# Kernel optimization log

Hardware: AMD Instinct MI355X
Metric: run time of the kernel (lower is better)

The kernel has to match this reference:

```python
import jax, jax.numpy as jnp
import numpy as np

B, L, H = 64, 512, 400          # batch, seq_len, encoder hidden (HeadSentinel(400))
EN, EL, NLAB = 256, 128, 128    # edge-node dim, edge-label hidden, num head_tags


def setup_inputs():
    key = jax.random.key(0)
    ks = jax.random.split(key, 16)
    g = lambda k, shape, s=0.05: jax.random.normal(k, shape, jnp.float32) * s
    return dict(
        memory_bank=jax.random.normal(ks[0], (B, L, H), jnp.float32),
        edge_heads=jax.random.randint(ks[1], (B, L), 0, L + 1, jnp.int32),
        edge_labels=jax.random.randint(ks[2], (B, L), 0, NLAB, jnp.int32),
        corefs=jax.random.randint(ks[3], (B, L), 0, L, jnp.int32),
        mask=jnp.ones((B, L), jnp.int32),
        sentinel=g(ks[4], (H,)),
        W_enh=g(ks[5], (H, EN)), b_enh=jnp.zeros((EN,), jnp.float32),
        W_enm=g(ks[6], (H, EN)), b_enm=jnp.zeros((EN,), jnp.float32),
        W_elh=g(ks[7], (H, EL)), b_elh=jnp.zeros((EL,), jnp.float32),
        W_elm=g(ks[8], (H, EL)), b_elm=jnp.zeros((EL,), jnp.float32),
        ba_U=g(ks[9], (EN, EN)), ba_Wd=g(ks[10], (EN,)), ba_We=g(ks[11], (EN,)),
        ba_b=jnp.zeros((), jnp.float32),
        lbl_U=g(ks[12], (NLAB, EL, EL)), lbl_Wl=g(ks[13], (NLAB, EL)),
        lbl_Wr=g(ks[14], (NLAB, EL)), lbl_b=jnp.zeros((NLAB,), jnp.float32),
    )


def _label_scores(elh_sel, elm, lbl_U, lbl_Wl, lbl_Wr, lbl_b):
    # Bilinear label scorer: [B, L1, NLAB]
    return (jnp.einsum('bld,nde,ble->bln', elh_sel, lbl_U, elm)
            + elh_sel @ lbl_Wl.T + elm @ lbl_Wr.T + lbl_b)


def reference(memory_bank, edge_heads, edge_labels, corefs, mask, sentinel,
              W_enh, b_enh, W_enm, b_enm, W_elh, b_elh, W_elm, b_elm,
              ba_U, ba_Wd, ba_We, ba_b, lbl_U, lbl_Wl, lbl_Wr, lbl_b):
    elu = jax.nn.elu
    Bsz = memory_bank.shape[0]
    # ---- add head sentinel (mask/heads/labels get a leading zero column) ----
    mb = jnp.concatenate([jnp.broadcast_to(sentinel, (Bsz, 1, sentinel.shape[0])), memory_bank], 1)
    z = jnp.zeros((Bsz, 1), jnp.int32)
    heads1 = jnp.concatenate([z, edge_heads], 1)    # [B, L1]
    labels1 = jnp.concatenate([z, edge_labels], 1)  # [B, L1]
    mask1 = jnp.concatenate([z, mask], 1)           # [B, L1]
    L1 = mb.shape[1]
    # ---- encode (Dropout is identity at inference) ----
    enh = elu(mb @ W_enh + b_enh)
    enm = elu(mb @ W_enm + b_enm)
    elh = elu(mb @ W_elh + b_elh)
    elm = elu(mb @ W_elm + b_elm)
    # ---- biaffine edge-node scores: s[b, head, mod] ----
    node_scores = (jnp.einsum('bhd,de,bme->bhm', enh, ba_U, enm)
                   + (enh @ ba_Wd)[:, :, None] + (enm @ ba_We)[:, None, :] + ba_b)
    # ---- loss ----
    mask2 = (mask1[:, :, None] + mask1[:, None, :]).astype(jnp.float32)
    node_ll = jax.nn.log_softmax(node_scores + jnp.log(mask2 + 1e-45), axis=1)
    elh_gold = jnp.take_along_axis(elh, heads1[:, :, None], axis=1)  # gather_nd(create_indices)
    lbl_ll = jax.nn.log_softmax(_label_scores(elh_gold, elm, lbl_U, lbl_Wl, lbl_Wr, lbl_b), axis=2)
    gold_node_ll = jnp.take_along_axis(node_ll, heads1[:, None, :], axis=1)[:, 0, :]  # ll[b, head[b,m], m]
    gold_lbl_ll = jnp.take_along_axis(lbl_ll, labels1[:, :, None], axis=2)[:, :, 0]   # ll[b, m, label[b,m]]
    node_nll = -jnp.sum(gold_node_ll[:, 1:])
    label_nll = -jnp.sum(gold_lbl_ll[:, 1:])
    # ---- decode ----
    dec = node_scores + jnp.diag(jnp.full((L1,), -jnp.inf))
    mm = (1.0 - mask1.astype(jnp.float32)) * (-1e8)
    dec = dec + mm[:, :, None] + mm[:, None, :]
    pred_heads = jnp.argmax(dec, axis=1)                              # [B, L1]
    elh_pred = jnp.take_along_axis(elh, pred_heads[:, :, None], axis=1)
    pred_lbl = jnp.max(_label_scores(elh_pred, elm, lbl_U, lbl_Wl, lbl_Wr, lbl_b), axis=2)
    return (pred_heads[:, 1:].astype(jnp.float32), pred_lbl[:, 1:],
            labels1.astype(jnp.float32), node_nll, label_nll)
```

## Files before the change

### kernel.cpp

```cpp
#include <hip/hip_runtime.h>
#include <hip/hip_bf16.h>

#define BB 64
#define LLEN 512
#define HH 400
#define L1 513
#define TT 32832
#define NE 768
#define KP 16640
#define PHW 4160
#define KPAD 416

typedef __attribute__((ext_vector_type(4))) float f32x4;
typedef __attribute__((ext_vector_type(8))) short bf16x8;
typedef unsigned int u32;
typedef __attribute__((address_space(1))) const u32* gptr_t;
typedef __attribute__((address_space(3))) u32* sptr_t;

__device__ inline unsigned short f2bf(float x){
  unsigned u = __float_as_uint(x);
  unsigned r = (u + 0x7fffu + ((u >> 16) & 1u)) >> 16;
  return (unsigned short)r;
}
__device__ inline unsigned cvtpk(float a, float b){
  unsigned r;
  asm("v_cvt_pk_bf16_f32 %0, %1, %2" : "=v"(r) : "v"(a), "v"(b));
  return r;
}
__device__ inline float bf2f(unsigned short h){
  return __uint_as_float(((unsigned)h) << 16);
}

__global__ __launch_bounds__(256) void k_init(const int* eh, const int* el, float* out,
                                              int* idx, int* labbuf){
  int t = blockIdx.x*256 + threadIdx.x;
  if (t < TT){
    int b = t / L1, m = t - b*L1;
    int lab = m ? el[b*LLEN + m - 1] : 0;
    int hd  = m ? eh[b*LLEN + m - 1] : 0;
    out[65536 + t] = (float)lab;
    labbuf[t] = lab;
    idx[t] = b*L1 + hd;
  }
  if (blockIdx.x == 0 && threadIdx.x < 2) out[98368 + threadIdx.x] = 0.f;
}

__global__ __launch_bounds__(256) void k_wcat(const float* Wenh,const float* benh,
    const float* Wenm,const float* benm,const float* Welh,const float* belh,
    const float* Welm,const float* belm, unsigned short* WH, unsigned short* WL,
    float* bcat){
  int g = blockIdx.x*256 + threadIdx.x;
  if (g < NE*KPAD){
    int n = g / KPAD, k = g - n*KPAD;
    float v = 0.f;
    if (k < HH){
      if (n < 256) v = Wenh[k*256 + n];
      else if (n < 512) v = Wenm[k*256 + n - 256];
      else if (n < 640) v = Welh[k*128 + n - 512];
      else v = Welm[k*128 + n - 640];
    }
    unsigned short h = f2bf(v);
    WH[g] = h;
    WL[g] = f2bf(v - bf2f(h));
  }
  if (g < NE){
    float v;
    if (g < 256) v = benh[g];
    else if (g < 512) v = benm[g - 256];
    else if (g < 640) v = belh[g - 512];
    else v = belm[g - 640];
    bcat[g] = v;
  }
}

__global__ __launch_bounds__(256) void k_wtt(const float* lblU, const float* Wl,
    const float* Wr, unsigned short* WtTp){
  int n = blockIdx.y;
  int kp = blockIdx.x*256 + threadIdx.x;
  if (kp >= KP) return;
  int p = kp / PHW; int q2 = kp - p*PHW; int dd = q2 >> 5; int j = q2 & 31; int e = p*32 + j;
  float v;
  if (dd < 128) v = lblU[(size_t)n*16384 + dd*128 + e];
  else if (dd == 128) v = Wl[n*128 + e];
  else v = Wr[n*128 + e];
  WtTp[(size_t)n*KP + kp] = f2bf(v);
}

#define INNER8(AS, BS) \
  _Pragma("unroll") \
  for (int kk = 0; kk < 8; kk++){ \
    float4 a0 = *(const float4*)&AS[kk][ty*8]; \
    float4 a1 = *(const float4*)&AS[kk][ty*8+4]; \
    float4 b0 = *(const float4*)&BS[kk][tx*8]; \
    float4 b1 = *(const float4*)&BS[kk][tx*8+4]; \
    float avv[8] = {a0.x,a0.y,a0.z,a0.w,a1.x,a1.y,a1.z,a1.w}; \
    float bvv[8] = {b0.x,b0.y,b0.z,b0.w,b1.x,b1.y,b1.z,b1.w}; \
    _Pragma("unroll") \
    for (int ii = 0; ii < 8; ii++) \
      _Pragma("unroll") \
      for (int jj = 0; jj < 8; jj++) \
        c_[ii][jj] += avv[ii]*bvv[jj]; \
  }

__global__ __launch_bounds__(512) void k_encm(const float* mb, const float* sent,
    const unsigned short* WH, const unsigned short* WL, const float* bcat, float* E){
  __shared__ __align__(16) unsigned char Bst[2][2][8192];
  int tid = threadIdx.x, w = tid >> 6, lane = tid & 63, c = lane & 15, q = lane >> 4;
  int tb0 = blockIdx.x*256 + w*32;
  int n0 = blockIdx.y*128;

  const float* ap[2];
  #pragma unroll
  for (int ms = 0; ms < 2; ms++){
    int row = tb0 + ms*16 + c;
    const float* p = sent;
    if (row < TT){
      int br = row / L1, mr = row - br*L1;
      if (mr) p = mb + (size_t)(br*LLEN + mr - 1)*HH;
    }
    ap[ms] = p;
  }

  int f = tid;
  int bn = ((f >> 6) << 4) + (f & 15);
  int bkq = (f >> 4) & 3;
  const char* srcH = (const char*)WH + (size_t)(n0 + bn)*(KPAD*2) + bkq*16;
  const char* srcL = (const char*)WL + (size_t)(n0 + bn)*(KPAD*2) + bkq*16;
  auto stageB = [&](int s){
    __builtin_amdgcn_global_load_lds((gptr_t)(srcH + (size_t)s*64),
        (sptr_t)(&Bst[s & 1][0][f*16]), 16, 0, 0);
    __builtin_amdgcn_global_load_lds((gptr_t)(srcL + (size_t)s*64),
        (sptr_t)(&Bst[s & 1][1][f*16]), 16, 0, 0);
  };

  float4 a0[2], a1[2];
  auto loadA = [&](int s){
    #pragma unroll
    for (int ms = 0; ms < 2; ms++){
      int k = s*32 + q*8;
      float4 v0 = make_float4(0.f,0.f,0.f,0.f), v1 = v0;
      if (k < HH){ v0 = *(const float4*)(ap[ms] + k); v1 = *(const float4*)(ap[ms] + k + 4); }
      a0[ms] = v0; a1[ms] = v1;
    }
  };
  stageB(0);
  loadA(0);

  f32x4 acc[2][8];
  #pragma unroll
  for (int ms = 0; ms < 2; ms++)
    #pragma unroll
    for (int ns = 0; ns < 8; ns++){ acc[ms][ns][0]=0.f; acc[ms][ns][1]=0.f; acc[ms][ns][2]=0.f; acc[ms][ns][3]=0.f; }

  for (int s = 0; s < 13; s++){
    asm volatile("s_waitcnt vmcnt(0)" ::: "memory");
    __builtin_amdgcn_sched_barrier(0);
    __builtin_amdgcn_s_barrier();
    __builtin_amdgcn_sched_barrier(0);
    if (s + 1 < 13) stageB(s + 1);
    bf16x8 Ah[2], Al[2];
    #pragma unroll
    for (int ms = 0; ms < 2; ms++){
      float v[8] = {a0[ms].x,a0[ms].y,a0[ms].z,a0[ms].w,a1[ms].x,a1[ms].y,a1[ms].z,a1[ms].w};
      union { unsigned u[4]; bf16x8 b; } uh, ul;
      float r[8];
      #pragma unroll
      for (int j = 0; j < 4; j++){
        unsigned h = cvtpk(v[2*j], v[2*j+1]);
        uh.u[j] = h;
        r[2*j]   = v[2*j]   - __uint_as_float((h & 0xffffu) << 16);
        r[2*j+1] = v[2*j+1] - __uint_as_float((h >> 16) << 16);
      }
      #pragma unroll
      for (int j = 0; j < 4; j++) ul.u[j] = cvtpk(r[2*j], r[2*j+1]);
      Ah[ms] = uh.b; Al[ms] = ul.b;
    }
    if (s + 1 < 13) loadA(s + 1);
    const char* bh = (const char*)&Bst[s & 1][0][0];
    const char* bl = (const char*)&Bst[s & 1][1][0];
    #pragma unroll
    for (int ns = 0; ns < 8; ns++){
      bf16x8 BH = *(const bf16x8*)(bh + ns*1024 + lane*16);
      bf16x8 BL = *(const bf16x8*)(bl + ns*1024 + lane*16);
      #pragma unroll
      for (int ms = 0; ms < 2; ms++){
        acc[ms][ns] = __builtin_amdgcn_mfma_f32_16x16x32_bf16(Ah[ms], BH, acc[ms][ns], 0, 0, 0);
        acc[ms][ns] = __builtin_amdgcn_mfma_f32_16x16x32_bf16(Ah[ms], BL, acc[ms][ns], 0, 0, 0);
        acc[ms][ns] = __builtin_amdgcn_mfma_f32_16x16x32_bf16(Al[ms], BH, acc[ms][ns], 0, 0, 0);
      }
    }
  }

  float bvv[8];
  #pragma unroll
  for (int ns = 0; ns < 8; ns++) bvv[ns] = bcat[n0 + ns*16 + c];
  #pragma unroll
  for (int ms = 0; ms < 2; ms++){
    #pragma unroll
    for (int i = 0; i < 4; i++){
      int row = tb0 + ms*16 + 4*q + i;
      if (row < TT){
        #pragma unroll
        for (int ns = 0; ns < 8; ns++){
          float t = acc[ms][ns][i] + bvv[ns];
          E[(size_t)row*NE + n0 + ns*16 + c] = t > 0.f ? t : expm1f(t);
        }
      }
    }
  }
}

__global__ __launch_bounds__(256) void k_t1(const float* E, const float* baU, float* T1){
  __shared__ float As[8][132];
  __shared__ float Bs[8][132];
  int tid = threadIdx.x, tx = tid & 15, ty = tid >> 4;
  int Mb = blockIdx.x * 128, n0 = blockIdx.y * 128;
  int ar = tid >> 1, akc = (tid & 1) * 4;
  int row = Mb + ar;
  bool aval = row < TT;
  const float* ap = E + (size_t)(aval ? row : 0)*NE;
  int bkr = tid >> 5, bnc = (tid & 31) * 4;
  float c_[8][8] = {};
  for (int k0 = 0; k0 < 256; k0 += 8){
    __syncthreads();
    float4 av = make_float4(0.f,0.f,0.f,0.f);
    if (aval) av = *(const float4*)(ap + k0 + akc);
    As[akc+0][ar] = av.x; As[akc+1][ar] = av.y; As[akc+2][ar] = av.z; As[akc+3][ar] = av.w;
    *(float4*)&Bs[bkr][bnc] = *(const float4*)(baU + (size_t)(k0 + bkr)*256 + n0 + bnc);
    __syncthreads();
    INNER8(As, Bs)
  }
  #pragma unroll
  for (int i = 0; i < 8; i++){
    int rr = Mb + ty*8 + i;
    if (rr < TT){
      float4 o0 = {c_[i][0],c_[i][1],c_[i][2],c_[i][3]};
      float4 o1 = {c_[i][4],c_[i][5],c_[i][6],c_[i][7]};
      *(float4*)&T1[(size_t)rr*256 + n0 + tx*8] = o0;
      *(float4*)&T1[(size_t)rr*256 + n0 + tx*8 + 4] = o1;
    }
  }
}

__global__ __launch_bounds__(256) void k_vecs(const float* E, const float* Wd,
    const float* We, const float* bab, float* dvec, float* evec){
  int w = threadIdx.x >> 6, lane = threadIdx.x & 63;
  int t = blockIdx.x*4 + w;
  const float* enh = E + (size_t)t*NE;
  const float* enm = enh + 256;
  float sd = 0.f, se = 0.f;
  for (int l = lane; l < 256; l += 64){ sd += enh[l]*Wd[l]; se += enm[l]*We[l]; }
  for (int o = 1; o < 64; o <<= 1){ sd += __shfl_xor(sd, o, 64); se += __shfl_xor(se, o, 64); }
  if (lane == 0){ dvec[t] = sd + bab[0]; evec[t] = se; }
}

__global__ __launch_bounds__(256) void k_ns(const float* T1, const float* E,
    const float* dvec, const float* evec, float* S){
  __shared__ float As[8][132];
  __shared__ float Bs[8][132];
  int tid = threadIdx.x, tx = tid & 15, ty = tid >> 4;
  int b = blockIdx.y;
  int tm = blockIdx.x / 5, tn = blockIdx.x - tm*5;
  int Mb = tm*128, n0 = tn*128;
  int ar = tid >> 1, akc = (tid & 1) * 4;
  int hrow = Mb + ar; bool aval = hrow < L1;
  const float* ap = T1 + ((size_t)b*L1 + (aval ? hrow : 0))*256;
  int mrow = n0 + ar; bool bval = mrow < L1;
  const float* bp = E + ((size_t)b*L1 + (bval ? mrow : 0))*NE + 256;
  float c_[8][8] = {};
  for (int k0 = 0; k0 < 256; k0 += 8){
    __syncthreads();
    float4 av = make_float4(0.f,0.f,0.f,0.f);
    float4 bv2 = make_float4(0.f,0.f,0.f,0.f);
    if (aval) av = *(const float4*)(ap + k0 + akc);
    if (bval) bv2 = *(const float4*)(bp + k0 + akc);
    As[akc+0][ar] = av.x; As[akc+1][ar] = av.y; As[akc+2][ar] = av.z; As[akc+3][ar] = av.w;
    Bs[akc+0][ar] = bv2.x; Bs[akc+1][ar] = bv2.y; Bs[akc+2][ar] = bv2.z; Bs[akc+3][ar] = bv2.w;
    __syncthreads();
    INNER8(As, Bs)
  }
  float dr[8], er[8];
  #pragma unroll
  for (int i = 0; i < 8; i++){ int h = Mb + ty*8 + i; dr[i] = (h < L1) ? dvec[b*L1 + h] : 0.f; }
  #pragma unroll
  for (int j = 0; j < 8; j++){ int m = n0 + tx*8 + j; er[j] = (m < L1) ? evec[b*L1 + m] : 0.f; }
  float* Sb = S + (size_t)b*L1*L1;
  #pragma unroll
  for (int i = 0; i < 8; i++){
    int h = Mb + ty*8 + i;
    if (h < L1){
      #pragma unroll
      for (int j = 0; j < 8; j++){
        int m = n0 + tx*8 + j;
        if (m < L1) Sb[(size_t)h*L1 + m] = c_[i][j] + dr[i] + er[j];
      }
    }
  }
}

__global__ __launch_bounds__(256) void k_nodecol(const float* S, const int* eh,
    const int* mask, float* out, int* idx){
  int b = blockIdx.y, mt = blockIdx.x;
  __shared__ float msk[L1];
  __shared__ float rM[8][32], rS[8][32], rG[8][32], rB[8][32];
  __shared__ int rH[8][32];
  __shared__ float npart[32];
  int tid = threadIdx.x; int c = tid & 31, r = tid >> 5;
  for (int h = tid; h < L1; h += 256) msk[h] = h ? (float)mask[b*LLEN + h - 1] : 0.f;
  __syncthreads();
  int m = mt*32 + c; bool valid = m < L1; int mc = valid ? m : (L1-1);
  float maskm = msk[mc];
  int gold = 0; if (valid && m) gold = eh[b*LLEN + m - 1];
  const float* Sb = S + (size_t)b*L1*L1;
  float Mx = -3.4e38f, Sm = 0.f, G = 0.f, Bv = -3.4e38f; int Bh = 0;
  for (int h = r; h < L1; h += 8){
    float s = Sb[(size_t)h*L1 + mc];
    float adj = s + ((msk[h] + maskm) > 1.5f ? 0.69314718055994531f : 0.f);
    float nm = fmaxf(Mx, adj);
    Sm = Sm * expf(Mx - nm) + expf(adj - nm);
    Mx = nm;
    if (h == gold) G = adj;
    float dv = (h == m) ? -3.4e38f : (s + (msk[h] > 0.5f ? 0.f : -1e8f));
    if (dv > Bv){ Bv = dv; Bh = h; }
  }
  rM[r][c] = Mx; rS[r][c] = Sm; rG[r][c] = G; rB[r][c] = Bv; rH[r][c] = Bh;
  __syncthreads();
  if (r == 0){
    float M0 = rM[0][c], S0 = rS[0][c], G0 = rG[0][c], B0 = rB[0][c]; int H0 = rH[0][c];
    for (int rr = 1; rr < 8; rr++){
      float m2 = rM[rr][c], s2 = rS[rr][c];
      float nm = fmaxf(M0, m2);
      S0 = S0*expf(M0 - nm) + s2*expf(m2 - nm); M0 = nm;
      G0 += rG[rr][c];
      float b2 = rB[rr][c]; int h2 = rH[rr][c];
      if (b2 > B0 || (b2 == B0 && h2 < H0)){ B0 = b2; H0 = h2; }
    }
    float nll = 0.f;
    if (valid && m >= 1) nll = (M0 + logf(S0)) - G0;
    npart[c] = nll;
    if (valid){
      idx[TT + b*L1 + m] = b*L1 + H0;
      if (m >= 1) out[b*LLEN + m - 1] = (float)H0;
    }
  }
  __syncthreads();
  if (tid == 0){
    float ssum = 0.f;
    for (int i2 = 0; i2 < 32; i2++) ssum += npart[i2];
    atomicAdd(out + 98368, ssum);
  }
}

__global__ __launch_bounds__(512, 1) void k_label(const float* E, const unsigned short* WtTp,
    const int* idx, const int* labbuf, const float* lblb, float* out){
  __shared__ __align__(16) unsigned char Bst[8*8192];
  __shared__ __align__(16) unsigned int xls[256*65];
  int tid = threadIdx.x;
  int w = tid >> 6, lane = tid & 63, c = lane & 15, q = lane >> 4;
  int wgrp = w & 3, khalf = w >> 2;
  int bx = blockIdx.x;
  bool pred = bx >= 128;
  int q0 = (bx & 127) * 256;
  int ibase = pred ? TT : 0;

  const char* gW = (const char*)WtTp;
  int f = tid;
  int bn = ((f >> 6) << 4) + (f & 15);
  int bkq = (f >> 4) & 3;
  const char* bsrc0 = gW + (size_t)bn*(KP*2) + (size_t)bkq*16;
  unsigned char* BbA = Bst;
  unsigned char* BbB = Bst + 4*8192;
  auto stage2 = [&](int s){
    __builtin_amdgcn_global_load_lds((gptr_t)(bsrc0 + (size_t)s*64),
        (sptr_t)(BbA + (s & 3)*8192 + f*16), 16, 0, 0);
    __builtin_amdgcn_global_load_lds((gptr_t)(bsrc0 + (size_t)(260 + s)*64),
        (sptr_t)(BbB + (s & 3)*8192 + f*16), 16, 0, 0);
  };
  stage2(0); stage2(1);

  {
    int tok = tid >> 1, half = tid & 1;
    int qq = q0 + tok;
    int trow = (qq >> 9)*L1 + (qq & 511) + 1;
    int g = idx[ibase + trow];
    const float* xr = E + (size_t)g*NE + 512 + half*64;
    unsigned* dstx = &xls[tok*65 + half*32];
    #pragma unroll
    for (int j = 0; j < 16; j++){
      float4 v = *(const float4*)(xr + j*4);
      dstx[2*j]   = cvtpk(v.x, v.y);
      dstx[2*j+1] = cvtpk(v.z, v.w);
    }
  }

  const float *yvb[4], *xvb[4];
  int tokl[4];
  #pragma unroll
  for (int ms = 0; ms < 4; ms++){
    int tl = (wgrp*4 + ms)*16 + c;
    tokl[ms] = tl;
    int qq = q0 + tl;
    int trow = (qq >> 9)*L1 + (qq & 511) + 1;
    int g = idx[ibase + trow];
    yvb[ms] = E + (size_t)trow*NE + 640 + 8*q;
    xvb[ms] = E + (size_t)g*NE + 512 + 8*q;
  }
  f32x4 acc[4][8];
  #pragma unroll
  for (int ms = 0; ms < 4; ms++)
    #pragma unroll
    for (int ns = 0; ns < 8; ns++){ acc[ms][ns][0]=0.f; acc[ms][ns][1]=0.f; acc[ms][ns][2]=0.f; acc[ms][ns][3]=0.f; }

  __syncthreads();

  const unsigned short* xsh = (const unsigned short*)xls;
  float xs0[4], xs1[4];
  #pragma unroll
  for (int ms = 0; ms < 4; ms++){
    xs0[ms] = bf2f(xsh[tokl[ms]*130]);
    xs1[ms] = bf2f(xsh[tokl[ms]*130 + 1]);
  }

  float yreg[4][8];
  for (int u = 0; u < 130; u++){
    if (u) { asm volatile("s_waitcnt vmcnt(0)" ::: "memory"); }
    __builtin_amdgcn_sched_barrier(0);
    __builtin_amdgcn_s_barrier();
    __builtin_amdgcn_sched_barrier(0);
    if (2*u + 2 < 260){ stage2(2*u + 2); stage2(2*u + 3); }
    int ph = (u >= 65);
    int d0 = 2*u - ph*130;
    if (d0 == 0){
      int e0 = (khalf*2 + ph) * 32;
      #pragma unroll
      for (int ms = 0; ms < 4; ms++){
        float4 v0 = *(const float4*)(yvb[ms] + e0);
        float4 v1 = *(const float4*)(yvb[ms] + e0 + 4);
        yreg[ms][0]=v0.x; yreg[ms][1]=v0.y; yreg[ms][2]=v0.z; yreg[ms][3]=v0.w;
        yreg[ms][4]=v1.x; yreg[ms][5]=v1.y; yreg[ms][6]=v1.z; yreg[ms][7]=v1.w;
      }
    }
    bf16x8 afr0[4], afr1[4];
    if (d0 < 128){
      #pragma unroll
      for (int ms = 0; ms < 4; ms++){
        float a0 = xs0[ms], a1 = xs1[ms];
        union { unsigned u[4]; bf16x8 v; } u0, u1;
        u0.u[0] = cvtpk(a0*yreg[ms][0], a0*yreg[ms][1]);
        u0.u[1] = cvtpk(a0*yreg[ms][2], a0*yreg[ms][3]);
        u0.u[2] = cvtpk(a0*yreg[ms][4], a0*yreg[ms][5]);
        u0.u[3] = cvtpk(a0*yreg[ms][6], a0*yreg[ms][7]);
        u1.u[0] = cvtpk(a1*yreg[ms][0], a1*yreg[ms][1]);
        u1.u[1] = cvtpk(a1*yreg[ms][2], a1*yreg[ms][3]);
        u1.u[2] = cvtpk(a1*yreg[ms][4], a1*yreg[ms][5]);
        u1.u[3] = cvtpk(a1*yreg[ms][6], a1*yreg[ms][7]);
        afr0[ms] = u0.v; afr1[ms] = u1.v;
      }
    } else {
      int e0 = (khalf*2 + ph) * 32;
      #pragma unroll
      for (int ms = 0; ms < 4; ms++){
        float4 u0f = *(const float4*)(xvb[ms] + e0);
        float4 u1f = *(const float4*)(xvb[ms] + e0 + 4);
        union { unsigned u[4]; bf16x8 v; } ux, uy;
        ux.u[0]=cvtpk(u0f.x,u0f.y); ux.u[1]=cvtpk(u0f.z,u0f.w);
        ux.u[2]=cvtpk(u1f.x,u1f.y); ux.u[3]=cvtpk(u1f.z,u1f.w);
        uy.u[0]=cvtpk(yreg[ms][0],yreg[ms][1]); uy.u[1]=cvtpk(yreg[ms][2],yreg[ms][3]);
        uy.u[2]=cvtpk(yreg[ms][4],yreg[ms][5]); uy.u[3]=cvtpk(yreg[ms][6],yreg[ms][7]);
        afr0[ms] = ux.v; afr1[ms] = uy.v;
      }
    }
    {
      int nd0 = 2*(u + 1) - ((u + 1 >= 65) ? 130 : 0);
      if (nd0 >= 128) nd0 = 0;
      #pragma unroll
      for (int ms = 0; ms < 4; ms++){
        xs0[ms] = bf2f(xsh[tokl[ms]*130 + nd0]);
        xs1[ms] = bf2f(xsh[tokl[ms]*130 + nd0 + 1]);
      }
    }
    const char* hb = (const char*)(khalf ? BbB : BbA);
    const char* bs0 = hb + ((2*u) & 3)*8192;
    const char* bs1 = hb + ((2*u + 1) & 3)*8192;
    #pragma unroll
    for (int ns = 0; ns < 8; ns++){
      bf16x8 bfr0 = *(const bf16x8*)(bs0 + ns*1024 + lane*16);
      bf16x8 bfr1 = *(const bf16x8*)(bs1 + ns*1024 + lane*16);
      #pragma unroll
      for (int ms = 0; ms < 4; ms++){
        acc[ms][ns] = __builtin_amdgcn_mfma_f32_16x16x32_bf16(afr0[ms], bfr0, acc[ms][ns], 0, 0, 0);
        acc[ms][ns] = __builtin_amdgcn_mfma_f32_16x16x32_bf16(afr1[ms], bfr1, acc[ms][ns], 0, 0, 0);
      }
    }
  }

  __syncthreads();
  float* cmb = (float*)xls;
  #pragma unroll
  for (int ms = 0; ms < 4; ms++){
    if (khalf == 1){
      #pragma unroll
      for (int ns = 0; ns < 8; ns++)
        *(f32x4*)&cmb[((wgrp*64 + lane)*8 + ((ns + lane) & 7))*4] = acc[ms][ns];
    }
    __syncthreads();
    if (khalf == 0){
      #pragma unroll
      for (int ns = 0; ns < 8; ns++){
        f32x4 t = *(const f32x4*)&cmb[((wgrp*64 + lane)*8 + ((ns + lane) & 7))*4];
        acc[ms][ns][0] += t[0]; acc[ms][ns][1] += t[1];
        acc[ms][ns][2] += t[2]; acc[ms][ns][3] += t[3];
      }
    }
    __syncthreads();
  }
  if (khalf == 1) return;

  float bv[8];
  #pragma unroll
  for (int ns = 0; ns < 8; ns++) bv[ns] = lblb[ns*16 + c];
  float part = 0.f;
  #pragma unroll
  for (int ms = 0; ms < 4; ms++){
    int tb = (wgrp*4 + ms)*16 + 4*q;
    float mx[4] = {-3.4e38f, -3.4e38f, -3.4e38f, -3.4e38f};
    #pragma unroll
    for (int ns = 0; ns < 8; ns++)
      #pragma unroll
      for (int i = 0; i < 4; i++){
        float v = acc[ms][ns][i] + bv[ns];
        mx[i] = fmaxf(mx[i], v);
      }
    #pragma unroll
    for (int o = 1; o < 16; o <<= 1)
      #pragma unroll
      for (int i = 0; i < 4; i++) mx[i] = fmaxf(mx[i], __shfl_xor(mx[i], o, 64));
    if (!pred){
      int lab[4];
      #pragma unroll
      for (int i = 0; i < 4; i++){
        int qq = q0 + tb + i;
        int trow = (qq >> 9)*L1 + (qq & 511) + 1;
        lab[i] = labbuf[trow];
      }
      float se[4] = {0.f,0.f,0.f,0.f}, gp[4] = {0.f,0.f,0.f,0.f};
      #pragma unroll
      for (int ns = 0; ns < 8; ns++)
        #pragma unroll
        for (int i = 0; i < 4; i++){
          float v = acc[ms][ns][i] + bv[ns];
          se[i] += expf(v - mx[i]);
          if (ns*16 + c == lab[i]) gp[i] += v;
        }
      #pragma unroll
      for (int o = 1; o < 16; o <<= 1)
        #pragma unroll
        for (int i = 0; i < 4; i++){ se[i] += __shfl_xor(se[i], o, 64); gp[i] += __shfl_xor(gp[i], o, 64); }
      if (c == 0){
        #pragma unroll
        for (int i = 0; i < 4; i++) part += mx[i] + logf(se[i]) - gp[i];
      }
    } else {
      if (c == 0){
        #pragma unroll
        for (int i = 0; i < 4; i++)
          out[32768 + q0 + tb + i] = mx[i];
      }
    }
  }
  if (!pred){
    for (int o = 1; o < 64; o <<= 1) part += __shfl_xor(part, o, 64);
    if (lane == 0) atomicAdd(out + 98369, part);
  }
}

extern "C" void kernel_launch(void* const* d_in, const int* in_sizes, int n_in,
                              void* d_out, int out_size, void* d_ws, size_t ws_size,
                              hipStream_t stream){
  const float* memory_bank = (const float*)d_in[0];
  const int* edge_heads = (const int*)d_in[1];
  const int* edge_labels = (const int*)d_in[2];
  const int* mask = (const int*)d_in[4];
  const float* sentinel = (const float*)d_in[5];
  const float* W_enh = (const float*)d_in[6];  const float* b_enh = (const float*)d_in[7];
  const float* W_enm = (const float*)d_in[8];  const float* b_enm = (const float*)d_in[9];
  const float* W_elh = (const float*)d_in[10]; const float* b_elh = (const float*)d_in[11];
  const float* W_elm = (const float*)d_in[12]; const float* b_elm = (const float*)d_in[13];
  const float* ba_U = (const float*)d_in[14];  const float* ba_Wd = (const float*)d_in[15];
  const float* ba_We = (const float*)d_in[16]; const float* ba_b = (const float*)d_in[17];
  const float* lbl_U = (const float*)d_in[18]; const float* lbl_Wl = (const float*)d_in[19];
  const float* lbl_Wr = (const float*)d_in[20]; const float* lbl_b = (const float*)d_in[21];
  float* out = (float*)d_out;

  char* wsc = (char*)d_ws;
  size_t o = 0;
  auto alloc = [&](size_t n){ o = (o + 255) & ~(size_t)255; void* pp = wsc + o; o += n; return pp; };
  float* E     = (float*)alloc((size_t)TT*NE*4);
  float* T1    = (float*)alloc((size_t)TT*256*4);
  float* S     = (float*)alloc((size_t)BB*L1*L1*4);
  unsigned short* WH = (unsigned short*)alloc((size_t)NE*KPAD*2);
  unsigned short* WL = (unsigned short*)alloc((size_t)NE*KPAD*2);
  float* bcat  = (float*)alloc((size_t)NE*4);
  unsigned short* WtTp = (unsigned short*)alloc((size_t)128*KP*2);
  float* dvec  = (float*)alloc((size_t)TT*4);
  float* evec  = (float*)alloc((size_t)TT*4);
  int*   idx   = (int*)alloc((size_t)2*TT*4);
  int*   labbuf= (int*)alloc((size_t)TT*4);

  k_init<<<dim3(129), 256, 0, stream>>>(edge_heads, edge_labels, out, idx, labbuf);
  k_wcat<<<dim3(1248), 256, 0, stream>>>(W_enh, b_enh, W_enm, b_enm, W_elh, b_elh, W_elm, b_elm, WH, WL, bcat);
  k_wtt<<<dim3(65, 128), 256, 0, stream>>>(lbl_U, lbl_Wl, lbl_Wr, WtTp);
  k_encm<<<dim3(129, 6), 512, 0, stream>>>(memory_bank, sentinel, WH, WL, bcat, E);
  k_t1<<<dim3(257, 2), 256, 0, stream>>>(E, ba_U, T1);
  k_vecs<<<dim3(8208), 256, 0, stream>>>(E, ba_Wd, ba_We, ba_b, dvec, evec);
  k_ns<<<dim3(25, 64), 256, 0, stream>>>(T1, E, dvec, evec, S);
  k_nodecol<<<dim3(17, 64), 256, 0, stream>>>(S, edge_heads, mask, out, idx);
  k_label<<<dim3(256), 512, 0, stream>>>(E, WtTp, idx, labbuf, lbl_b, out);
}
```

Baseline: 840.1 us.

## Move biaffine GEMMs to bf16x3 split MFMA with double-buffered LDS staging

Rewrites the two scalar-FP32 biaffine GEMMs (E·U giving T1, and T1·enmᵀ giving node scores) to use bf16 MFMA 16x16x32 instructions. Each FP32 operand is split into a high and a low bf16 part and three products are accumulated to keep near-FP32 accuracy. A new pre-kernel transposes ba_U and splits it once. Tiles are double-buffered in LDS, using global_load_lds for U and in-register conversion for E. This adds conversion arithmetic and three times the MFMA count in exchange for matrix-core throughput.

```diff
diff --git a/kernel.cpp b/kernel.cpp
--- a/kernel.cpp
+++ b/kernel.cpp
@@ -73,6 +73,16 @@
   }
 }
 
+__global__ __launch_bounds__(256) void k_wu(const float* baU, unsigned short* UH,
+    unsigned short* UL){
+  int g = blockIdx.x*256 + threadIdx.x;
+  int n = g >> 8, k = g & 255;
+  float v = baU[k*256 + n];
+  unsigned short h = f2bf(v);
+  UH[g] = h;
+  UL[g] = f2bf(v - bf2f(h));
+}
+
 __global__ __launch_bounds__(256) void k_wtt(const float* lblU, const float* Wl,
     const float* Wr, unsigned short* WtTp){
   int n = blockIdx.y;
@@ -86,22 +96,6 @@
   WtTp[(size_t)n*KP + kp] = f2bf(v);
 }
 
-#define INNER8(AS, BS) \
-  _Pragma("unroll") \
-  for (int kk = 0; kk < 8; kk++){ \
-    float4 a0 = *(const float4*)&AS[kk][ty*8]; \
-    float4 a1 = *(const float4*)&AS[kk][ty*8+4]; \
-    float4 b0 = *(const float4*)&BS[kk][tx*8]; \
-    float4 b1 = *(const float4*)&BS[kk][tx*8+4]; \
-    float avv[8] = {a0.x,a0.y,a0.z,a0.w,a1.x,a1.y,a1.z,a1.w}; \
-    float bvv[8] = {b0.x,b0.y,b0.z,b0.w,b1.x,b1.y,b1.z,b1.w}; \
-    _Pragma("unroll") \
-    for (int ii = 0; ii < 8; ii++) \
-      _Pragma("unroll") \
-      for (int jj = 0; jj < 8; jj++) \
-        c_[ii][jj] += avv[ii]*bvv[jj]; \
-  }
-
 __global__ __launch_bounds__(512) void k_encm(const float* mb, const float* sent,
     const unsigned short* WH, const unsigned short* WL, const float* bcat, float* E){
   __shared__ __align__(16) unsigned char Bst[2][2][8192];
@@ -210,34 +204,100 @@
   }
 }
 
-__global__ __launch_bounds__(256) void k_t1(const float* E, const float* baU, float* T1){
-  __shared__ float As[8][132];
-  __shared__ float Bs[8][132];
-  int tid = threadIdx.x, tx = tid & 15, ty = tid >> 4;
-  int Mb = blockIdx.x * 128, n0 = blockIdx.y * 128;
-  int ar = tid >> 1, akc = (tid & 1) * 4;
-  int row = Mb + ar;
-  bool aval = row < TT;
-  const float* ap = E + (size_t)(aval ? row : 0)*NE;
-  int bkr = tid >> 5, bnc = (tid & 31) * 4;
-  float c_[8][8] = {};
-  for (int k0 = 0; k0 < 256; k0 += 8){
-    __syncthreads();
-    float4 av = make_float4(0.f,0.f,0.f,0.f);
-    if (aval) av = *(const float4*)(ap + k0 + akc);
-    As[akc+0][ar] = av.x; As[akc+1][ar] = av.y; As[akc+2][ar] = av.z; As[akc+3][ar] = av.w;
-    *(float4*)&Bs[bkr][bnc] = *(const float4*)(baU + (size_t)(k0 + bkr)*256 + n0 + bnc);
-    __syncthreads();
-    INNER8(As, Bs)
-  }
-  #pragma unroll
-  for (int i = 0; i < 8; i++){
-    int rr = Mb + ty*8 + i;
-    if (rr < TT){
-      float4 o0 = {c_[i][0],c_[i][1],c_[i][2],c_[i][3]};
-      float4 o1 = {c_[i][4],c_[i][5],c_[i][6],c_[i][7]};
-      *(float4*)&T1[(size_t)rr*256 + n0 + tx*8] = o0;
-      *(float4*)&T1[(size_t)rr*256 + n0 + tx*8 + 4] = o1;
+__global__ __launch_bounds__(256) void k_t1m(const float* E, const unsigned short* UH,
+    const unsigned short* UL, float* T1){
+  __shared__ __align__(16) unsigned char Bst[2][2][8192];
+  int tid = threadIdx.x, w = tid >> 6, lane = tid & 63, c = lane & 15, q = lane >> 4;
+  int tb0 = blockIdx.x*128 + w*32;
+  int n0 = blockIdx.y*128;
+
+  const float* ap[2];
+  #pragma unroll
+  for (int ms = 0; ms < 2; ms++){
+    int row = tb0 + ms*16 + c;
+    ap[ms] = E + (size_t)(row < TT ? row : 0)*NE;
+  }
+
+  auto stageB = [&](int s){
+    #pragma unroll
+    for (int i = 0; i < 2; i++){
+      int f = i*256 + tid;
+      int n = n0 + ((f >> 6) << 4) + (f & 15);
+      int kq = (f >> 4) & 3;
+      __builtin_amdgcn_global_load_lds((gptr_t)((const char*)UH + (size_t)n*512 + (size_t)s*64 + kq*16),
+          (sptr_t)(&Bst[s & 1][0][f*16]), 16, 0, 0);
+      __builtin_amdgcn_global_load_lds((gptr_t)((const char*)UL + (size_t)n*512 + (size_t)s*64 + kq*16),
+          (sptr_t)(&Bst[s & 1][1][f*16]), 16, 0, 0);
+    }
+  };
+
+  float4 a0[2], a1[2];
+  auto loadA = [&](int s){
+    #pragma unroll
+    for (int ms = 0; ms < 2; ms++){
+      int k = s*32 + q*8;
+      a0[ms] = *(const float4*)(ap[ms] + k);
+      a1[ms] = *(const float4*)(ap[ms] + k + 4);
+    }
+  };
+  stageB(0);
+  loadA(0);
+
+  f32x4 acc[2][8];
+  #pragma unroll
+  for (int ms = 0; ms < 2; ms++)
+    #pragma unroll
+    for (int ns = 0; ns < 8; ns++){ acc[ms][ns][0]=0.f; acc[ms][ns][1]=0.f; acc[ms][ns][2]=0.f; acc[ms][ns][3]=0.f; }
+
+  for (int s = 0; s < 8; s++){
+    asm volatile("s_waitcnt vmcnt(0)" ::: "memory");
+    __builtin_amdgcn_sched_barrier(0);
+    __builtin_amdgcn_s_barrier();
+    __builtin_amdgcn_sched_barrier(0);
+    if (s + 1 < 8) stageB(s + 1);
+    bf16x8 Ah[2], Al[2];
+    #pragma unroll
+    for (int ms = 0; ms < 2; ms++){
+      float v[8] = {a0[ms].x,a0[ms].y,a0[ms].z,a0[ms].w,a1[ms].x,a1[ms].y,a1[ms].z,a1[ms].w};
+      union { unsigned u[4]; bf16x8 b; } uh, ul;
+      float r[8];
+      #pragma unroll
+      for (int j = 0; j < 4; j++){
+        unsigned h = cvtpk(v[2*j], v[2*j+1]);
+        uh.u[j] = h;
+        r[2*j]   = v[2*j]   - __uint_as_float((h & 0xffffu) << 16);
+        r[2*j+1] = v[2*j+1] - __uint_as_float((h >> 16) << 16);
+      }
+      #pragma unroll
+      for (int j = 0; j < 4; j++) ul.u[j] = cvtpk(r[2*j], r[2*j+1]);
+      Ah[ms] = uh.b; Al[ms] = ul.b;
+    }
+    if (s + 1 < 8) loadA(s + 1);
+    const char* bh = (const char*)&Bst[s & 1][0][0];
+    const char* bl = (const char*)&Bst[s & 1][1][0];
+    #pragma unroll
+    for (int ns = 0; ns < 8; ns++){
+      bf16x8 BH = *(const bf16x8*)(bh + ns*1024 + lane*16);
+      bf16x8 BL = *(const bf16x8*)(bl + ns*1024 + lane*16);
+      #pragma unroll
+      for (int ms = 0; ms < 2; ms++){
+        acc[ms][ns] = __builtin_amdgcn_mfma_f32_16x16x32_bf16(Ah[ms], BH, acc[ms][ns], 0, 0, 0);
+        acc[ms][ns] = __builtin_amdgcn_mfma_f32_16x16x32_bf16(Ah[ms], BL, acc[ms][ns], 0, 0, 0);
+        acc[ms][ns] = __builtin_amdgcn_mfma_f32_16x16x32_bf16(Al[ms], BH, acc[ms][ns], 0, 0, 0);
+      }
+    }
+  }
+
+  #pragma unroll
+  for (int ms = 0; ms < 2; ms++){
+    #pragma unroll
+    for (int i = 0; i < 4; i++){
+      int row = tb0 + ms*16 + 4*q + i;
+      if (row < TT){
+        #pragma unroll
+        for (int ns = 0; ns < 8; ns++)
+          T1[(size_t)row*256 + n0 + ns*16 + c] = acc[ms][ns][i];
+      }
     }
   }
 }
@@ -254,45 +314,127 @@
   if (lane == 0){ dvec[t] = sd + bab[0]; evec[t] = se; }
 }
 
-__global__ __launch_bounds__(256) void k_ns(const float* T1, const float* E,
+__global__ __launch_bounds__(256) void k_nsm(const float* T1, const float* E,
     const float* dvec, const float* evec, float* S){
-  __shared__ float As[8][132];
-  __shared__ float Bs[8][132];
-  int tid = threadIdx.x, tx = tid & 15, ty = tid >> 4;
+  __shared__ __align__(16) unsigned char Bst[2][2][8192];
+  int tid = threadIdx.x, w = tid >> 6, lane = tid & 63, c = lane & 15, q = lane >> 4;
   int b = blockIdx.y;
   int tm = blockIdx.x / 5, tn = blockIdx.x - tm*5;
   int Mb = tm*128, n0 = tn*128;
-  int ar = tid >> 1, akc = (tid & 1) * 4;
-  int hrow = Mb + ar; bool aval = hrow < L1;
-  const float* ap = T1 + ((size_t)b*L1 + (aval ? hrow : 0))*256;
-  int mrow = n0 + ar; bool bval = mrow < L1;
-  const float* bp = E + ((size_t)b*L1 + (bval ? mrow : 0))*NE + 256;
-  float c_[8][8] = {};
-  for (int k0 = 0; k0 < 256; k0 += 8){
+  int tb0 = Mb + w*32;
+
+  const float* ap[2];
+  #pragma unroll
+  for (int ms = 0; ms < 2; ms++){
+    int h = tb0 + ms*16 + c;
+    int hc = h < L1 ? h : L1 - 1;
+    ap[ms] = T1 + ((size_t)b*L1 + hc)*256;
+  }
+
+  auto stageB = [&](int s, int buf){
+    int k0 = s*32;
+    #pragma unroll
+    for (int i = 0; i < 2; i++){
+      int f = i*256 + tid;
+      int mc = n0 + ((f >> 6) << 4) + (f & 15);
+      int kq = (f >> 4) & 3;
+      int mcc = mc < L1 ? mc : L1 - 1;
+      const float* src = E + ((size_t)b*L1 + mcc)*NE + 256 + k0 + kq*8;
+      float4 v0 = *(const float4*)src;
+      float4 v1 = *(const float4*)(src + 4);
+      float v[8] = {v0.x,v0.y,v0.z,v0.w,v1.x,v1.y,v1.z,v1.w};
+      union { unsigned u[4]; uint4 u4; } uh, ul;
+      float r[8];
+      #pragma unroll
+      for (int j = 0; j < 4; j++){
+        unsigned h = cvtpk(v[2*j], v[2*j+1]);
+        uh.u[j] = h;
+        r[2*j]   = v[2*j]   - __uint_as_float((h & 0xffffu) << 16);
+        r[2*j+1] = v[2*j+1] - __uint_as_float((h >> 16) << 16);
+      }
+      #pragma unroll
+      for (int j = 0; j < 4; j++) ul.u[j] = cvtpk(r[2*j], r[2*j+1]);
+      *(uint4*)&Bst[buf][0][f*16] = uh.u4;
+      *(uint4*)&Bst[buf][1][f*16] = ul.u4;
+    }
+  };
+
+  float4 a0[2], a1[2];
+  auto loadA = [&](int s){
+    #pragma unroll
+    for (int ms = 0; ms < 2; ms++){
+      int k = s*32 + q*8;
+      a0[ms] = *(const float4*)(ap[ms] + k);
+      a1[ms] = *(const float4*)(ap[ms] + k + 4);
+    }
+  };
+
+  stageB(0, 0);
+  loadA(0);
+
+  f32x4 acc[2][8];
+  #pragma unroll
+  for (int ms = 0; ms < 2; ms++)
+    #pragma unroll
+    for (int ns = 0; ns < 8; ns++){ acc[ms][ns][0]=0.f; acc[ms][ns][1]=0.f; acc[ms][ns][2]=0.f; acc[ms][ns][3]=0.f; }
+
+  __syncthreads();
+
+  for (int s = 0; s < 8; s++){
+    if (s + 1 < 8) stageB(s + 1, (s + 1) & 1);
+    bf16x8 Ah[2], Al[2];
+    #pragma unroll
+    for (int ms = 0; ms < 2; ms++){
+      float v[8] = {a0[ms].x,a0[ms].y,a0[ms].z,a0[ms].w,a1[ms].x,a1[ms].y,a1[ms].z,a1[ms].w};
+      union { unsigned u[4]; bf16x8 b; } uh, ul;
+      float r[8];
+      #pragma unroll
+      for (int j = 0; j < 4; j++){
+        unsigned h = cvtpk(v[2*j], v[2*j+1]);
+        uh.u[j] = h;
+        r[2*j]   = v[2*j]   - __uint_as_float((h & 0xffffu) << 16);
+        r[2*j+1] = v[2*j+1] - __uint_as_float((h >> 16) << 16);
+      }
+      #pragma unroll
+      for (int j = 0; j < 4; j++) ul.u[j] = cvtpk(r[2*j], r[2*j+1]);
+      Ah[ms] = uh.b; Al[ms] = ul.b;
+    }
+    if (s + 1 < 8) loadA(s + 1);
+    const char* bh = (const char*)&Bst[s & 1][0][0];
+    const char* bl = (const char*)&Bst[s & 1][1][0];
+    #pragma unroll
+    for (int ns = 0; ns < 8; ns++){
+      bf16x8 BH = *(const bf16x8*)(bh + ns*1024 + lane*16);
+      bf16x8 BL = *(const bf16x8*)(bl + ns*1024 + lane*16);
+      #pragma unroll
+      for (int ms = 0; ms < 2; ms++){
+        acc[ms][ns] = __builtin_amdgcn_mfma_f32_16x16x32_bf16(Ah[ms], BH, acc[ms][ns], 0, 0, 0);
+        acc[ms][ns] = __builtin_amdgcn_mfma_f32_16x16x32_bf16(Ah[ms], BL, acc[ms][ns], 0, 0, 0);
+        acc[ms][ns] = __builtin_amdgcn_mfma_f32_16x16x32_bf16(Al[ms], BH, acc[ms][ns], 0, 0, 0);
+      }
+    }
     __syncthreads();
-    float4 av = make_float4(0.f,0.f,0.f,0.f);
-    float4 bv2 = make_float4(0.f,0.f,0.f,0.f);
-    if (aval) av = *(const float4*)(ap + k0 + akc);
-    if (bval) bv2 = *(const float4*)(bp + k0 + akc);
-    As[akc+0][ar] = av.x; As[akc+1][ar] = av.y; As[akc+2][ar] = av.z; As[akc+3][ar] = av.w;
-    Bs[akc+0][ar] = bv2.x; Bs[akc+1][ar] = bv2.y; Bs[akc+2][ar] = bv2.z; Bs[akc+3][ar] = bv2.w;
-    __syncthreads();
-    INNER8(As, Bs)
-  }
-  float dr[8], er[8];
-  #pragma unroll
-  for (int i = 0; i < 8; i++){ int h = Mb + ty*8 + i; dr[i] = (h < L1) ? dvec[b*L1 + h] : 0.f; }
-  #pragma unroll
-  for (int j = 0; j < 8; j++){ int m = n0 + tx*8 + j; er[j] = (m < L1) ? evec[b*L1 + m] : 0.f; }
+  }
+
+  float er[8];
+  #pragma unroll
+  for (int ns = 0; ns < 8; ns++){
+    int m = n0 + ns*16 + c;
+    er[ns] = (m < L1) ? evec[b*L1 + m] : 0.f;
+  }
   float* Sb = S + (size_t)b*L1*L1;
   #pragma unroll
-  for (int i = 0; i < 8; i++){
-    int h = Mb + ty*8 + i;
-    if (h < L1){
-      #pragma unroll
-      for (int j = 0; j < 8; j++){
-        int m = n0 + tx*8 + j;
-        if (m < L1) Sb[(size_t)h*L1 + m] = c_[i][j] + dr[i] + er[j];
+  for (int ms = 0; ms < 2; ms++){
+    #pragma unroll
+    for (int i = 0; i < 4; i++){
+      int h = tb0 + ms*16 + 4*q + i;
+      if (h < L1){
+        float dv = dvec[b*L1 + h];
+        #pragma unroll
+        for (int ns = 0; ns < 8; ns++){
+          int m = n0 + ns*16 + c;
+          if (m < L1) Sb[(size_t)h*L1 + m] = acc[ms][ns][i] + dv + er[ns];
+        }
       }
     }
   }
@@ -600,6 +742,8 @@
   float* S     = (float*)alloc((size_t)BB*L1*L1*4);
   unsigned short* WH = (unsigned short*)alloc((size_t)NE*KPAD*2);
   unsigned short* WL = (unsigned short*)alloc((size_t)NE*KPAD*2);
+  unsigned short* UH = (unsigned short*)alloc((size_t)256*256*2);
+  unsigned short* UL = (unsigned short*)alloc((size_t)256*256*2);
   float* bcat  = (float*)alloc((size_t)NE*4);
   unsigned short* WtTp = (unsigned short*)alloc((size_t)128*KP*2);
   float* dvec  = (float*)alloc((size_t)TT*4);
@@ -609,11 +753,12 @@
 
   k_init<<<dim3(129), 256, 0, stream>>>(edge_heads, edge_labels, out, idx, labbuf);
   k_wcat<<<dim3(1248), 256, 0, stream>>>(W_enh, b_enh, W_enm, b_enm, W_elh, b_elh, W_elm, b_elm, WH, WL, bcat);
+  k_wu<<<dim3(256), 256, 0, stream>>>(ba_U, UH, UL);
   k_wtt<<<dim3(65, 128), 256, 0, stream>>>(lbl_U, lbl_Wl, lbl_Wr, WtTp);
   k_encm<<<dim3(129, 6), 512, 0, stream>>>(memory_bank, sentinel, WH, WL, bcat, E);
-  k_t1<<<dim3(257, 2), 256, 0, stream>>>(E, ba_U, T1);
+  k_t1m<<<dim3(257, 2), 256, 0, stream>>>(E, UH, UL, T1);
   k_vecs<<<dim3(8208), 256, 0, stream>>>(E, ba_Wd, ba_We, ba_b, dvec, evec);
-  k_ns<<<dim3(25, 64), 256, 0, stream>>>(T1, E, dvec, evec, S);
+  k_nsm<<<dim3(25, 64), 256, 0, stream>>>(T1, E, dvec, evec, S);
   k_nodecol<<<dim3(17, 64), 256, 0, stream>>>(S, edge_heads, mask, out, idx);
   k_label<<<dim3(256), 512, 0, stream>>>(E, WtTp, idx, labbuf, lbl_b, out);
 }
```

After: 699.9 us. 16.7% less time.
